# Kernel optimization log

Hardware: AMD Instinct MI355X
Metric: run time of the kernel (lower is better)

The kernel has to match this reference:

```python
import jax, jax.numpy as jnp
import numpy as np

WS = (4, 4, 4)  # window shape (wd, wh, ww)
EPS = 1e-5


def _layernorm(x, g, b):
    mu = jnp.mean(x, axis=-1, keepdims=True)
    var = jnp.mean(jnp.square(x - mu), axis=-1, keepdims=True)
    return (x - mu) * jax.lax.rsqrt(var + EPS) * g + b


def _partition(x, ws):
    # x: [B, D, H, W, C] -> [num_windows, wd*wh*ww, C]
    B, D, H, W, C = x.shape
    x = x.reshape(B, D // ws[0], ws[0], H // ws[1], ws[1], W // ws[2], ws[2], C)
    x = jnp.transpose(x, (0, 1, 3, 5, 2, 4, 6, 7))
    return x.reshape(-1, ws[0] * ws[1] * ws[2], C)


def _merge(win, shape, ws):
    B, D, H, W, C = shape
    x = win.reshape(B, D // ws[0], H // ws[1], W // ws[2], ws[0], ws[1], ws[2], C)
    x = jnp.transpose(x, (0, 1, 4, 2, 5, 3, 6, 7))
    return x.reshape(B, D, H, W, C)


def setup_inputs() -> dict:
    key = jax.random.key(0)
    ks = jax.random.split(key, 8)
    B, D, H, W, C = 2, 32, 64, 64, 96
    nh, kd = 4, 24
    s = 0.02
    return {
        "x": jax.random.normal(ks[0], (B, D, H, W, C), jnp.float32),
        "ln1_g": jnp.ones((C,), jnp.float32),
        "ln1_b": jnp.zeros((C,), jnp.float32),
        "wq": jax.random.normal(ks[1], (C, nh, kd), jnp.float32) * s,
        "bq": jnp.zeros((nh, kd), jnp.float32),
        "wk": jax.random.normal(ks[2], (C, nh, kd), jnp.float32) * s,
        "bk": jnp.zeros((nh, kd), jnp.float32),
        "wv": jax.random.normal(ks[3], (C, nh, kd), jnp.float32) * s,
        "bv": jnp.zeros((nh, kd), jnp.float32),
        "wo": jax.random.normal(ks[4], (nh, kd, C), jnp.float32) * s,
        "bo": jnp.zeros((C,), jnp.float32),
        "ln2_g": jnp.ones((C,), jnp.float32),
        "ln2_b": jnp.zeros((C,), jnp.float32),
        "w1": jax.random.normal(ks[5], (C, 4 * C), jnp.float32) * s,
        "b1": jnp.zeros((4 * C,), jnp.float32),
        "w2": jax.random.normal(ks[6], (4 * C, C), jnp.float32) * s,
        "b2": jnp.zeros((C,), jnp.float32),
    }


def reference(x, ln1_g, ln1_b, wq, bq, wk, bk, wv, bv, wo, bo,
              ln2_g, ln2_b, w1, b1, w2, b2):
    shape = x.shape  # [B, D, H, W, C]; dims chosen divisible by WS -> pad is a no-op
    kd = wq.shape[-1]
    shortcut = x
    h = _layernorm(x, ln1_g, ln1_b)
    win = _partition(h, WS)  # [n, L, C], L = 64
    # Keras MultiHeadAttention (inference, dropout off)
    q = jnp.einsum("nlc,chd->nlhd", win, wq) + bq
    k = jnp.einsum("nlc,chd->nlhd", win, wk) + bk
    v = jnp.einsum("nlc,chd->nlhd", win, wv) + bv
    scores = jnp.einsum("nlhd,nmhd->nhlm", q, k) / jnp.sqrt(jnp.float32(kd))
    attn = jax.nn.softmax(scores, axis=-1)
    o = jnp.einsum("nhlm,nmhd->nlhd", attn, v)
    out = jnp.einsum("nlhd,hdc->nlc", o, wo) + bo
    x = shortcut + _merge(out, shape, WS)
    shortcut = x
    h = _layernorm(x, ln2_g, ln2_b)
    h = jax.nn.gelu(h @ w1 + b1, approximate=False)  # TF keras 'gelu' is exact
    h = h @ w2 + b2
    return shortcut + h
```

## Files before the change

### kernel.cpp

```cpp
#include <hip/hip_runtime.h>
#include <hip/hip_bf16.h>

typedef __attribute__((ext_vector_type(8))) short short8;
typedef __attribute__((ext_vector_type(4))) short short4b;
typedef __attribute__((ext_vector_type(4))) float f32x4;
typedef unsigned short ushort_t;

#define NTOK 262144

__device__ __forceinline__ ushort_t f2bf(float f){
  __hip_bfloat16 h = __float2bfloat16(f);
  return *reinterpret_cast<ushort_t*>(&h);
}
__device__ __forceinline__ float bf2f(ushort_t u){
  union { unsigned int i; float f; } v; v.i = ((unsigned int)u) << 16; return v.f;
}
__device__ __forceinline__ float fast_rcp(float x){
  float r; asm("v_rcp_f32 %0, %1" : "=v"(r) : "v"(x)); return r;
}
__device__ __forceinline__ float gelu_f(float x){
  float e = __expf(-1.702f * x);
  return x * fast_rcp(1.0f + e);
}
__device__ __forceinline__ void bar_lds(){
  asm volatile("s_waitcnt lgkmcnt(0)" ::: "memory");
  __builtin_amdgcn_s_barrier();
  __builtin_amdgcn_sched_barrier(0);
}
__device__ __forceinline__ void bar_cnt5(){
  asm volatile("s_waitcnt vmcnt(5) lgkmcnt(0)" ::: "memory");
  __builtin_amdgcn_s_barrier();
  __builtin_amdgcn_sched_barrier(0);
}
__device__ __forceinline__ void bar_cnt0(){
  asm volatile("s_waitcnt vmcnt(0) lgkmcnt(0)" ::: "memory");
  __builtin_amdgcn_s_barrier();
  __builtin_amdgcn_sched_barrier(0);
}
__device__ __forceinline__ void gl_lds16(const ushort_t* g, ushort_t* l){
  __builtin_amdgcn_global_load_lds(
      (const __attribute__((address_space(1))) void*)g,
      (__attribute__((address_space(3))) void*)l, 16, 0, 0);
}

template<int NT>
__device__ __forceinline__ void stage_w(const ushort_t* __restrict__ src,
                                        int src_stride, ushort_t (*dst)[104], int tid)
{
  #pragma unroll
  for (int it = 0; it < (1248 + NT - 1) / NT; ++it) {
    int u = tid + it * NT;
    if (u < 1248) {
      int row = u / 13, c16 = u % 13;
      const ushort_t* sp = src + row * src_stride + ((c16 == 12) ? 0 : c16 * 8);
      gl_lds16(sp, &dst[0][0] + (size_t)(u & ~63) * 8);
    }
  }
}

__device__ __forceinline__ void stage_wp(const ushort_t* __restrict__ src,
                                         int src_stride, ushort_t* __restrict__ dst, int tid)
{
  #pragma unroll
  for (int it = 0; it < 5; ++it) {
    int u = tid + it * 256;
    int row = u / 13, c16 = u % 13;
    const ushort_t* sp = src + row * src_stride + ((c16 >= 12) ? 0 : c16 * 8);
    gl_lds16(sp, dst + (size_t)(u & ~63) * 8);
  }
}

__global__ __launch_bounds__(256) void prep_kernel(
    const float* __restrict__ wq, const float* __restrict__ wk, const float* __restrict__ wv,
    const float* __restrict__ wo, const float* __restrict__ w1, const float* __restrict__ w2,
    const float* __restrict__ bq, const float* __restrict__ bk, const float* __restrict__ bv,
    ushort_t* __restrict__ Wqkv, ushort_t* __restrict__ Wo,
    ushort_t* __restrict__ W1, ushort_t* __restrict__ W2, float* __restrict__ biasq)
{
  const float qs = 0.20412414523193150818f;
  int i = blockIdx.x * 256 + threadIdx.x;
  if (i < 27648) {
    int j = i / 96, c = i % 96;
    int s = j / 96, rem = j % 96;
    const float* src = (s == 0) ? wq : (s == 1) ? wk : wv;
    float val = src[c * 96 + rem];
    if (s == 0) val *= qs;
    Wqkv[j * 96 + c] = f2bf(val);
  } else if (i < 36864) {
    int ii = i - 27648;
    int c = ii / 96, hd = ii % 96;
    Wo[ii] = f2bf(wo[hd * 96 + c]);
  } else if (i < 73728) {
    int ii = i - 36864;
    int j = ii / 96, c = ii % 96;
    W1[ii] = f2bf(w1[c * 384 + j]);
  } else if (i < 110592) {
    int ii = i - 73728;
    int c = ii / 384, j = ii % 384;
    W2[ii] = f2bf(w2[j * 96 + c]);
  } else if (i < 110880) {
    int j = i - 110592;
    int s = j / 96, rem = j % 96;
    const float* src = (s == 0) ? bq : (s == 1) ? bk : bv;
    float val = src[rem];
    if (s == 0) val *= qs;
    biasq[j] = val;
  }
}

__global__ __launch_bounds__(256, 2) void fat_kernel(
    const float* __restrict__ x, const float* __restrict__ g, const float* __restrict__ b,
    const ushort_t* __restrict__ Wqkv, const float* __restrict__ biasq,
    const ushort_t* __restrict__ Wo, const float* __restrict__ bo,
    ushort_t* __restrict__ x2b)
{
  __shared__ ushort_t regionA[20480];
  __shared__ ushort_t Vt[4][32][72];
  __shared__ ushort_t Ws[96][104];
  ushort_t (*hbt)[104]   = reinterpret_cast<ushort_t(*)[104]>(regionA);
  ushort_t (*QK)[216]    = reinterpret_cast<ushort_t(*)[216]>(regionA + 64 * 104);
  ushort_t (*Pb)[64][72] = reinterpret_cast<ushort_t(*)[64][72]>(regionA);
  ushort_t (*O_lds)[104] = reinterpret_cast<ushort_t(*)[104]>(regionA);

  int tid = threadIdx.x;
  int n = blockIdx.x;
  int wq_ = n & 15, hq = (n >> 4) & 15, rest = n >> 8;
  int dq = rest & 7, bb_ = rest >> 3;
  int base = bb_ * 131072 + dq * 16384 + hq * 256 + wq_ * 4;
  #define TOK(s) (base + ((s) >> 4) * 4096 + (((s) >> 2) & 3) * 64 + ((s) & 3))

  stage_w<256>(Wqkv, 96, Ws, tid);

  {
    int s = tid >> 2, qr = tid & 3;
    const float* xp = x + (size_t)TOK(s) * 96 + qr * 24;
    f32x4 v[6];
    float sm = 0.f, sq = 0.f;
    #pragma unroll
    for (int i = 0; i < 6; i++) {
      v[i] = *reinterpret_cast<const f32x4*>(xp + i * 4);
      #pragma unroll
      for (int j = 0; j < 4; j++) { sm += v[i][j]; sq += v[i][j] * v[i][j]; }
    }
    sm += __shfl_xor(sm, 1); sq += __shfl_xor(sq, 1);
    sm += __shfl_xor(sm, 2); sq += __shfl_xor(sq, 2);
    float mean = sm * (1.0f / 96.0f);
    float var  = sq * (1.0f / 96.0f) - mean * mean;
    float rstd = rsqrtf(var + 1e-5f);
    #pragma unroll
    for (int i8 = 0; i8 < 3; i8++) {
      short8 pk;
      #pragma unroll
      for (int j = 0; j < 8; j++) {
        int c = qr * 24 + i8 * 8 + j;
        pk[j] = (short)f2bf((v[(i8 * 8 + j) >> 2][(i8 * 8 + j) & 3] - mean) * rstd * g[c] + b[c]);
      }
      *reinterpret_cast<short8*>(&hbt[s][qr * 24 + i8 * 8]) = pk;
    }
  }
  __syncthreads();

  int w = tid >> 6, lane = tid & 63, g16 = lane >> 4, l15 = lane & 15;
  short8 af[3];
  #pragma unroll
  for (int ks = 0; ks < 3; ks++)
    af[ks] = *reinterpret_cast<const short8*>(&hbt[w * 16 + l15][ks * 32 + g16 * 8]);

  for (int grp = 0; grp < 3; ++grp) {
    f32x4 acc[6];
    #pragma unroll
    for (int j = 0; j < 6; j++) acc[j] = (f32x4){0.f, 0.f, 0.f, 0.f};
    __builtin_amdgcn_s_setprio(1);
    #pragma unroll
    for (int j = 0; j < 6; j++)
      #pragma unroll
      for (int ks = 0; ks < 3; ks++) {
        short8 wfr = *reinterpret_cast<const short8*>(&Ws[j * 16 + l15][ks * 32 + g16 * 8]);
        acc[j] = __builtin_amdgcn_mfma_f32_16x16x32_bf16(wfr, af[ks], acc[j], 0, 0, 0);
      }
    __builtin_amdgcn_s_setprio(0);
    bar_lds();
    if (grp < 2) stage_w<256>(Wqkv + (grp + 1) * 9216, 96, Ws, tid);
    else         stage_w<256>(Wo, 96, Ws, tid);
    if (grp < 2) {
      #pragma unroll
      for (int j = 0; j < 6; j++) {
        int c0 = grp * 96 + j * 16 + g16 * 4;
        f32x4 bb4 = *reinterpret_cast<const f32x4*>(&biasq[c0]);
        unsigned lo = (unsigned)f2bf(acc[j][0] + bb4[0]) | ((unsigned)f2bf(acc[j][1] + bb4[1]) << 16);
        unsigned hi = (unsigned)f2bf(acc[j][2] + bb4[2]) | ((unsigned)f2bf(acc[j][3] + bb4[3]) << 16);
        uint2 pk; pk.x = lo; pk.y = hi;
        *reinterpret_cast<uint2*>(&QK[w * 16 + l15][c0]) = pk;
      }
    } else {
      #pragma unroll
      for (int j = 0; j < 6; j++) {
        int c0 = j * 16 + g16 * 4;
        f32x4 bb4 = *reinterpret_cast<const f32x4*>(&biasq[192 + c0]);
        #pragma unroll
        for (int r = 0; r < 4; r++) {
          int vcol = c0 + r;
          int h2 = vcol / 24, d2 = vcol - h2 * 24;
          Vt[h2][d2][w * 16 + l15] = f2bf(acc[j][r] + bb4[r]);
        }
      }
    }
    __syncthreads();
  }

  int h = w;
  short8 kf[4], qf[4];
  const short8 z8 = {0, 0, 0, 0, 0, 0, 0, 0};
  #pragma unroll
  for (int i = 0; i < 4; i++) {
    qf[i] = (g16 < 3) ? *(const short8*)&QK[i * 16 + l15][h * 24 + g16 * 8]      : z8;
    kf[i] = (g16 < 3) ? *(const short8*)&QK[i * 16 + l15][96 + h * 24 + g16 * 8] : z8;
  }
  f32x4 st[4][4];
  __builtin_amdgcn_s_setprio(1);
  #pragma unroll
  for (int tm = 0; tm < 4; tm++)
    #pragma unroll
    for (int tn = 0; tn < 4; tn++)
      st[tm][tn] = __builtin_amdgcn_mfma_f32_16x16x32_bf16(kf[tm], qf[tn],
                    (f32x4){0.f, 0.f, 0.f, 0.f}, 0, 0, 0);
  __builtin_amdgcn_s_setprio(0);
  bar_lds();

  #pragma unroll
  for (int tn = 0; tn < 4; tn++) {
    float m = st[0][tn][0];
    #pragma unroll
    for (int tm = 0; tm < 4; tm++)
      #pragma unroll
      for (int r = 0; r < 4; r++) m = fmaxf(m, st[tm][tn][r]);
    m = fmaxf(m, __shfl_xor(m, 16));
    m = fmaxf(m, __shfl_xor(m, 32));
    float sum = 0.f;
    #pragma unroll
    for (int tm = 0; tm < 4; tm++)
      #pragma unroll
      for (int r = 0; r < 4; r++) {
        float e = __expf(st[tm][tn][r] - m);
        st[tm][tn][r] = e;
        sum += e;
      }
    sum += __shfl_xor(sum, 16);
    sum += __shfl_xor(sum, 32);
    float inv = fast_rcp(sum);
    int q = tn * 16 + l15;
    #pragma unroll
    for (int tm = 0; tm < 4; tm++) {
      unsigned lo = (unsigned)f2bf(st[tm][tn][0] * inv) | ((unsigned)f2bf(st[tm][tn][1] * inv) << 16);
      unsigned hi = (unsigned)f2bf(st[tm][tn][2] * inv) | ((unsigned)f2bf(st[tm][tn][3] * inv) << 16);
      uint2 pk; pk.x = lo; pk.y = hi;
      *(uint2*)&Pb[h][q][tm * 16 + g16 * 4] = pk;
    }
  }

  f32x4 oacc[4][2];
  #pragma unroll
  for (int qt = 0; qt < 4; qt++)
    #pragma unroll
    for (int dt = 0; dt < 2; dt++) oacc[qt][dt] = (f32x4){0.f, 0.f, 0.f, 0.f};
  __builtin_amdgcn_s_setprio(1);
  #pragma unroll
  for (int ks = 0; ks < 2; ks++) {
    short8 vb[2];
    #pragma unroll
    for (int dt = 0; dt < 2; dt++)
      vb[dt] = *(const short8*)&Vt[h][dt * 16 + l15][ks * 32 + g16 * 8];
    #pragma unroll
    for (int qt = 0; qt < 4; qt++) {
      short8 pa = *(const short8*)&Pb[h][qt * 16 + l15][ks * 32 + g16 * 8];
      #pragma unroll
      for (int dt = 0; dt < 2; dt++)
        oacc[qt][dt] = __builtin_amdgcn_mfma_f32_16x16x32_bf16(pa, vb[dt], oacc[qt][dt], 0, 0, 0);
    }
  }
  __builtin_amdgcn_s_setprio(0);

  __syncthreads();
  #pragma unroll
  for (int qt = 0; qt < 4; qt++)
    #pragma unroll
    for (int dt = 0; dt < 2; dt++) {
      int d = dt * 16 + l15;
      if (d < 24) {
        #pragma unroll
        for (int r = 0; r < 4; r++)
          O_lds[qt * 16 + g16 * 4 + r][h * 24 + d] = f2bf(oacc[qt][dt][r]);
      }
    }
  __syncthreads();

  f32x4 pacc[6];
  #pragma unroll
  for (int nt = 0; nt < 6; nt++) pacc[nt] = (f32x4){0.f, 0.f, 0.f, 0.f};
  __builtin_amdgcn_s_setprio(1);
  #pragma unroll
  for (int ks = 0; ks < 3; ks++) {
    short8 pa = *(const short8*)&O_lds[w * 16 + l15][ks * 32 + g16 * 8];
    #pragma unroll
    for (int nt = 0; nt < 6; nt++) {
      short8 wb = *reinterpret_cast<const short8*>(&Ws[nt * 16 + l15][ks * 32 + g16 * 8]);
      pacc[nt] = __builtin_amdgcn_mfma_f32_16x16x32_bf16(wb, pa, pacc[nt], 0, 0, 0);
    }
  }
  __builtin_amdgcn_s_setprio(0);
  {
    size_t t = (size_t)TOK(w * 16 + l15);
    #pragma unroll
    for (int nt = 0; nt < 6; nt++) {
      int c0 = nt * 16 + g16 * 4;
      f32x4 bo4 = *reinterpret_cast<const f32x4*>(&bo[c0]);
      f32x4 xr  = *reinterpret_cast<const f32x4*>(&x[t * 96 + c0]);
      float v0 = pacc[nt][0] + bo4[0] + xr[0];
      float v1 = pacc[nt][1] + bo4[1] + xr[1];
      float v2 = pacc[nt][2] + bo4[2] + xr[2];
      float v3 = pacc[nt][3] + bo4[3] + xr[3];
      unsigned lo = (unsigned)f2bf(v0) | ((unsigned)f2bf(v1) << 16);
      unsigned hi = (unsigned)f2bf(v2) | ((unsigned)f2bf(v3) << 16);
      uint2 pk; pk.x = lo; pk.y = hi;
      *reinterpret_cast<uint2*>(&x2b[t * 96 + c0]) = pk;
    }
  }
  #undef TOK
}

__device__ __forceinline__ void ln_to_lds_b(const ushort_t* __restrict__ xrow_base,
    const float* __restrict__ gg, const float* __restrict__ bb,
    ushort_t (*hbt)[104], int tid)
{
  int row = tid >> 1, half = tid & 1;
  const ushort_t* xp = xrow_base + (size_t)row * 96 + half * 48;
  short8 vv[6];
  #pragma unroll
  for (int i = 0; i < 6; i++) vv[i] = *reinterpret_cast<const short8*>(xp + i * 8);
  float v[48];
  float s = 0.f, sq = 0.f;
  #pragma unroll
  for (int i = 0; i < 6; i++)
    #pragma unroll
    for (int j = 0; j < 8; j++) {
      float f = bf2f((ushort_t)vv[i][j]);
      v[i * 8 + j] = f; s += f; sq += f * f;
    }
  s  += __shfl_xor(s, 1);
  sq += __shfl_xor(sq, 1);
  float mean = s * (1.0f / 96.0f);
  float var  = sq * (1.0f / 96.0f) - mean * mean;
  float rstd = rsqrtf(var + 1e-5f);
  #pragma unroll
  for (int i8 = 0; i8 < 6; i8++) {
    short8 pk;
    #pragma unroll
    for (int j = 0; j < 8; j++) {
      int c = half * 48 + i8 * 8 + j;
      pk[j] = (short)f2bf((v[i8 * 8 + j] - mean) * rstd * gg[c] + bb[c]);
    }
    *reinterpret_cast<short8*>(&hbt[row][half * 48 + i8 * 8]) = pk;
  }
}

__global__ __launch_bounds__(256, 2) void mlp2_kernel(
    const ushort_t* __restrict__ x2b, const float* __restrict__ g, const float* __restrict__ b,
    const ushort_t* __restrict__ W1t, const float* __restrict__ b1,
    const ushort_t* __restrict__ W2t, const float* __restrict__ b2,
    float* __restrict__ out)
{
  __shared__ ushort_t smem[128][104];
  __shared__ ushort_t WsA[10240];
  __shared__ ushort_t WsB[10240];
  __shared__ float bias1[384];
  __shared__ float bias2[96];
  int tid = threadIdx.x;
  size_t r0 = (size_t)blockIdx.x * 128;

  stage_wp(W1t, 96, WsA, tid);
  stage_wp(W2t, 384, WsB, tid);
  bias1[tid] = b1[tid];
  if (tid < 128) bias1[256 + tid] = b1[256 + tid];
  if (tid < 96)  bias2[tid] = b2[tid];
  ln_to_lds_b(x2b + r0 * 96, g, b, smem, tid);

  int w = tid >> 6, lane = tid & 63, g16 = lane >> 4, l15 = lane & 15;
  short8 af[2][3];
  #pragma unroll
  for (int mi = 0; mi < 2; mi++)
    #pragma unroll
    for (int ks = 0; ks < 3; ks++)
      af[mi][ks] = *reinterpret_cast<const short8*>(&smem[w * 32 + mi * 16 + l15][ks * 32 + g16 * 8]);
  __builtin_amdgcn_sched_barrier(0);

  f32x4 oacc[6][2];
  #pragma unroll
  for (int nt = 0; nt < 6; nt++) { oacc[nt][0] = (f32x4){0.f,0.f,0.f,0.f}; oacc[nt][1] = (f32x4){0.f,0.f,0.f,0.f}; }

  for (int cc = 0; cc < 4; ++cc) {
    bar_cnt5();
    f32x4 acc[6][2];
    #pragma unroll
    for (int nt = 0; nt < 6; nt++) { acc[nt][0] = (f32x4){0.f,0.f,0.f,0.f}; acc[nt][1] = (f32x4){0.f,0.f,0.f,0.f}; }
    __builtin_amdgcn_s_setprio(1);
    #pragma unroll
    for (int nt = 0; nt < 6; nt++)
      #pragma unroll
      for (int ks = 0; ks < 3; ks++) {
        short8 wfr = *reinterpret_cast<const short8*>(&WsA[(nt * 16 + l15) * 104 + ks * 32 + g16 * 8]);
        acc[nt][0] = __builtin_amdgcn_mfma_f32_16x16x32_bf16(wfr, af[0][ks], acc[nt][0], 0, 0, 0);
        acc[nt][1] = __builtin_amdgcn_mfma_f32_16x16x32_bf16(wfr, af[1][ks], acc[nt][1], 0, 0, 0);
      }
    __builtin_amdgcn_s_setprio(0);
    #pragma unroll
    for (int nt = 0; nt < 6; nt++) {
      f32x4 bb4 = *reinterpret_cast<const f32x4*>(&bias1[cc * 96 + nt * 16 + g16 * 4]);
      #pragma unroll
      for (int mi = 0; mi < 2; mi++) {
        float g0 = gelu_f(acc[nt][mi][0] + bb4[0]);
        float g1 = gelu_f(acc[nt][mi][1] + bb4[1]);
        float g2 = gelu_f(acc[nt][mi][2] + bb4[2]);
        float g3 = gelu_f(acc[nt][mi][3] + bb4[3]);
        unsigned lo = (unsigned)f2bf(g0) | ((unsigned)f2bf(g1) << 16);
        unsigned hi = (unsigned)f2bf(g2) | ((unsigned)f2bf(g3) << 16);
        uint2 pk; pk.x = lo; pk.y = hi;
        *reinterpret_cast<uint2*>(&smem[w * 32 + mi * 16 + l15][nt * 16 + g16 * 4]) = pk;
      }
    }
    short8 a2[2][3];
    #pragma unroll
    for (int mi = 0; mi < 2; mi++)
      #pragma unroll
      for (int ks = 0; ks < 3; ks++)
        a2[mi][ks] = *reinterpret_cast<const short8*>(&smem[w * 32 + mi * 16 + l15][ks * 32 + g16 * 8]);
    bar_lds();
    if (cc < 3) stage_wp(W1t + (cc + 1) * 9216, 96, WsA, tid);
    if (cc < 3) bar_cnt5(); else bar_cnt0();
    __builtin_amdgcn_s_setprio(1);
    #pragma unroll
    for (int nt = 0; nt < 6; nt++)
      #pragma unroll
      for (int ks = 0; ks < 3; ks++) {
        short8 wfr = *reinterpret_cast<const short8*>(&WsB[(nt * 16 + l15) * 104 + ks * 32 + g16 * 8]);
        oacc[nt][0] = __builtin_amdgcn_mfma_f32_16x16x32_bf16(wfr, a2[0][ks], oacc[nt][0], 0, 0, 0);
        oacc[nt][1] = __builtin_amdgcn_mfma_f32_16x16x32_bf16(wfr, a2[1][ks], oacc[nt][1], 0, 0, 0);
      }
    __builtin_amdgcn_s_setprio(0);
    if (cc < 3) {
      bar_lds();
      stage_wp(W2t + (cc + 1) * 96, 384, WsB, tid);
    }
  }

  #pragma unroll
  for (int nt = 0; nt < 6; nt++) {
    int c0 = nt * 16 + g16 * 4;
    f32x4 bb4 = *reinterpret_cast<const f32x4*>(&bias2[c0]);
    #pragma unroll
    for (int mi = 0; mi < 2; mi++) {
      size_t row = r0 + w * 32 + mi * 16 + l15;
      short4b rr = *reinterpret_cast<const short4b*>(&x2b[row * 96 + c0]);
      f32x4 o;
      #pragma unroll
      for (int r = 0; r < 4; r++) o[r] = oacc[nt][mi][r] + bb4[r] + bf2f((ushort_t)rr[r]);
      *reinterpret_cast<f32x4*>(&out[row * 96 + c0]) = o;
    }
  }
}

extern "C" void kernel_launch(void* const* d_in, const int* in_sizes, int n_in,
                              void* d_out, int out_size, void* d_ws, size_t ws_size,
                              hipStream_t stream)
{
  (void)in_sizes; (void)n_in; (void)out_size; (void)ws_size;
  const float* x    = (const float*)d_in[0];
  const float* ln1g = (const float*)d_in[1];
  const float* ln1b = (const float*)d_in[2];
  const float* wq   = (const float*)d_in[3];
  const float* bq   = (const float*)d_in[4];
  const float* wk   = (const float*)d_in[5];
  const float* bk   = (const float*)d_in[6];
  const float* wv   = (const float*)d_in[7];
  const float* bv   = (const float*)d_in[8];
  const float* wo   = (const float*)d_in[9];
  const float* bo   = (const float*)d_in[10];
  const float* ln2g = (const float*)d_in[11];
  const float* ln2b = (const float*)d_in[12];
  const float* w1   = (const float*)d_in[13];
  const float* b1   = (const float*)d_in[14];
  const float* w2   = (const float*)d_in[15];
  const float* b2   = (const float*)d_in[16];

  char* ws = (char*)d_ws;
  ushort_t* x2b  = (ushort_t*)(ws);
  char* wsw      = ws + 50331648;
  ushort_t* Wqkv = (ushort_t*)(wsw);
  ushort_t* Wo   = (ushort_t*)(wsw + 55296);
  ushort_t* W1   = (ushort_t*)(wsw + 55296 + 18432);
  ushort_t* W2   = (ushort_t*)(wsw + 55296 + 18432 + 73728);
  float*    biasq= (float*)   (wsw + 55296 + 18432 + 73728 + 73728);

  prep_kernel<<<434, 256, 0, stream>>>(wq, wk, wv, wo, w1, w2, bq, bk, bv,
                                       Wqkv, Wo, W1, W2, biasq);
  fat_kernel<<<4096, 256, 0, stream>>>(x, ln1g, ln1b, Wqkv, biasq, Wo, bo, x2b);
  mlp2_kernel<<<NTOK / 128, 256, 0, stream>>>(x2b, ln2g, ln2b, W1, b1, W2, b2, (float*)d_out);
}
```

Measured before the change: 183.3 us.

## Double-buffer QKV/Wo weight halves in LDS with vmcnt-based pipelined staging

Replaces the single padded 96x104 weight tile with two unpadded 48x96 half-tile buffers. Each half is staged with global_load_lds two steps ahead and waited on with a partial vmcnt barrier, so weight loads overlap the QKV projection MFMAs. It also drops the initial __syncthreads after LayerNorm, makes QK alias hbt in a smaller region, and swaps some __syncthreads for lighter custom barriers. Removing the padding may bring LDS bank conflicts on fragment reads. The hbt/QK aliasing and the counter-based waits are fragile correctness points.

```diff
diff --git a/kernel.cpp b/kernel.cpp
--- a/kernel.cpp
+++ b/kernel.cpp
@@ -27,6 +27,11 @@
   __builtin_amdgcn_s_barrier();
   __builtin_amdgcn_sched_barrier(0);
 }
+__device__ __forceinline__ void bar_cnt2(){
+  asm volatile("s_waitcnt vmcnt(2) lgkmcnt(0)" ::: "memory");
+  __builtin_amdgcn_s_barrier();
+  __builtin_amdgcn_sched_barrier(0);
+}
 __device__ __forceinline__ void bar_cnt5(){
   asm volatile("s_waitcnt vmcnt(5) lgkmcnt(0)" ::: "memory");
   __builtin_amdgcn_s_barrier();
@@ -43,19 +48,13 @@
       (__attribute__((address_space(3))) void*)l, 16, 0, 0);
 }
 
-template<int NT>
-__device__ __forceinline__ void stage_w(const ushort_t* __restrict__ src,
-                                        int src_stride, ushort_t (*dst)[104], int tid)
-{
-  #pragma unroll
-  for (int it = 0; it < (1248 + NT - 1) / NT; ++it) {
-    int u = tid + it * NT;
-    if (u < 1248) {
-      int row = u / 13, c16 = u % 13;
-      const ushort_t* sp = src + row * src_stride + ((c16 == 12) ? 0 : c16 * 8);
-      gl_lds16(sp, &dst[0][0] + (size_t)(u & ~63) * 8);
-    }
-  }
+__device__ __forceinline__ void stage_half(const ushort_t* __restrict__ src,
+                                           ushort_t* __restrict__ dst, int tid)
+{
+  gl_lds16(src + (size_t)tid * 8, dst + (size_t)(tid & ~63) * 8);
+  gl_lds16(src + (size_t)(tid + 256) * 8, dst + (size_t)((tid + 256) & ~63) * 8);
+  if (tid < 64)
+    gl_lds16(src + (size_t)(tid + 512) * 8, dst + (size_t)512 * 8);
 }
 
 __device__ __forceinline__ void stage_wp(const ushort_t* __restrict__ src,
@@ -114,11 +113,11 @@
     const ushort_t* __restrict__ Wo, const float* __restrict__ bo,
     ushort_t* __restrict__ x2b)
 {
-  __shared__ ushort_t regionA[20480];
+  __shared__ ushort_t regionA[18432];
   __shared__ ushort_t Vt[4][32][72];
-  __shared__ ushort_t Ws[96][104];
+  __shared__ ushort_t WsH[2][4608];
   ushort_t (*hbt)[104]   = reinterpret_cast<ushort_t(*)[104]>(regionA);
-  ushort_t (*QK)[216]    = reinterpret_cast<ushort_t(*)[216]>(regionA + 64 * 104);
+  ushort_t (*QK)[200]    = reinterpret_cast<ushort_t(*)[200]>(regionA);
   ushort_t (*Pb)[64][72] = reinterpret_cast<ushort_t(*)[64][72]>(regionA);
   ushort_t (*O_lds)[104] = reinterpret_cast<ushort_t(*)[104]>(regionA);
 
@@ -129,7 +128,8 @@
   int base = bb_ * 131072 + dq * 16384 + hq * 256 + wq_ * 4;
   #define TOK(s) (base + ((s) >> 4) * 4096 + (((s) >> 2) & 3) * 64 + ((s) & 3))
 
-  stage_w<256>(Wqkv, 96, Ws, tid);
+  stage_half(Wqkv, WsH[0], tid);
+  stage_half(Wqkv + 4608, WsH[1], tid);
 
   {
     int s = tid >> 2, qr = tid & 3;
@@ -158,55 +158,64 @@
       *reinterpret_cast<short8*>(&hbt[s][qr * 24 + i8 * 8]) = pk;
     }
   }
-  __syncthreads();
 
   int w = tid >> 6, lane = tid & 63, g16 = lane >> 4, l15 = lane & 15;
   short8 af[3];
   #pragma unroll
   for (int ks = 0; ks < 3; ks++)
     af[ks] = *reinterpret_cast<const short8*>(&hbt[w * 16 + l15][ks * 32 + g16 * 8]);
-
+  __builtin_amdgcn_sched_barrier(0);
+
+  int hidx = 0;
   for (int grp = 0; grp < 3; ++grp) {
-    f32x4 acc[6];
-    #pragma unroll
-    for (int j = 0; j < 6; j++) acc[j] = (f32x4){0.f, 0.f, 0.f, 0.f};
-    __builtin_amdgcn_s_setprio(1);
-    #pragma unroll
-    for (int j = 0; j < 6; j++)
-      #pragma unroll
-      for (int ks = 0; ks < 3; ks++) {
-        short8 wfr = *reinterpret_cast<const short8*>(&Ws[j * 16 + l15][ks * 32 + g16 * 8]);
-        acc[j] = __builtin_amdgcn_mfma_f32_16x16x32_bf16(wfr, af[ks], acc[j], 0, 0, 0);
-      }
-    __builtin_amdgcn_s_setprio(0);
-    bar_lds();
-    if (grp < 2) stage_w<256>(Wqkv + (grp + 1) * 9216, 96, Ws, tid);
-    else         stage_w<256>(Wo, 96, Ws, tid);
-    if (grp < 2) {
-      #pragma unroll
-      for (int j = 0; j < 6; j++) {
-        int c0 = grp * 96 + j * 16 + g16 * 4;
-        f32x4 bb4 = *reinterpret_cast<const f32x4*>(&biasq[c0]);
-        unsigned lo = (unsigned)f2bf(acc[j][0] + bb4[0]) | ((unsigned)f2bf(acc[j][1] + bb4[1]) << 16);
-        unsigned hi = (unsigned)f2bf(acc[j][2] + bb4[2]) | ((unsigned)f2bf(acc[j][3] + bb4[3]) << 16);
-        uint2 pk; pk.x = lo; pk.y = hi;
-        *reinterpret_cast<uint2*>(&QK[w * 16 + l15][c0]) = pk;
-      }
-    } else {
-      #pragma unroll
-      for (int j = 0; j < 6; j++) {
-        int c0 = j * 16 + g16 * 4;
-        f32x4 bb4 = *reinterpret_cast<const f32x4*>(&biasq[192 + c0]);
+    for (int half = 0; half < 2; ++half) {
+      const ushort_t* buf = WsH[hidx & 1];
+      bar_cnt2();
+      f32x4 acc[3];
+      #pragma unroll
+      for (int jj = 0; jj < 3; jj++) acc[jj] = (f32x4){0.f, 0.f, 0.f, 0.f};
+      __builtin_amdgcn_s_setprio(1);
+      #pragma unroll
+      for (int jj = 0; jj < 3; jj++)
         #pragma unroll
-        for (int r = 0; r < 4; r++) {
-          int vcol = c0 + r;
-          int h2 = vcol / 24, d2 = vcol - h2 * 24;
-          Vt[h2][d2][w * 16 + l15] = f2bf(acc[j][r] + bb4[r]);
+        for (int ks = 0; ks < 3; ks++) {
+          short8 wfr = *reinterpret_cast<const short8*>(&buf[(jj * 16 + l15) * 96 + ks * 32 + g16 * 8]);
+          acc[jj] = __builtin_amdgcn_mfma_f32_16x16x32_bf16(wfr, af[ks], acc[jj], 0, 0, 0);
         }
-      }
-    }
-    __syncthreads();
-  }
+      __builtin_amdgcn_s_setprio(0);
+      bar_lds();
+      if (hidx < 6) {
+        const ushort_t* s2 = (hidx + 2 < 6) ? Wqkv + (size_t)(hidx + 2) * 4608
+                                            : Wo + (size_t)(hidx - 4) * 4608;
+        stage_half(s2, WsH[hidx & 1], tid);
+      }
+      if (grp < 2) {
+        #pragma unroll
+        for (int jj = 0; jj < 3; jj++) {
+          int c0 = grp * 96 + (half * 3 + jj) * 16 + g16 * 4;
+          f32x4 bb4 = *reinterpret_cast<const f32x4*>(&biasq[c0]);
+          unsigned lo = (unsigned)f2bf(acc[jj][0] + bb4[0]) | ((unsigned)f2bf(acc[jj][1] + bb4[1]) << 16);
+          unsigned hi = (unsigned)f2bf(acc[jj][2] + bb4[2]) | ((unsigned)f2bf(acc[jj][3] + bb4[3]) << 16);
+          uint2 pk; pk.x = lo; pk.y = hi;
+          *reinterpret_cast<uint2*>(&QK[w * 16 + l15][c0]) = pk;
+        }
+      } else {
+        #pragma unroll
+        for (int jj = 0; jj < 3; jj++) {
+          int c0 = (half * 3 + jj) * 16 + g16 * 4;
+          f32x4 bb4 = *reinterpret_cast<const f32x4*>(&biasq[192 + c0]);
+          #pragma unroll
+          for (int r = 0; r < 4; r++) {
+            int vcol = c0 + r;
+            int h2 = vcol / 24, d2 = vcol - h2 * 24;
+            Vt[h2][d2][w * 16 + l15] = f2bf(acc[jj][r] + bb4[r]);
+          }
+        }
+      }
+      hidx++;
+    }
+  }
+  bar_lds();
 
   int h = w;
   short8 kf[4], qf[4];
@@ -280,7 +289,7 @@
   }
   __builtin_amdgcn_s_setprio(0);
 
-  __syncthreads();
+  bar_lds();
   #pragma unroll
   for (int qt = 0; qt < 4; qt++)
     #pragma unroll
@@ -292,7 +301,7 @@
           O_lds[qt * 16 + g16 * 4 + r][h * 24 + d] = f2bf(oacc[qt][dt][r]);
       }
     }
-  __syncthreads();
+  bar_cnt0();
 
   f32x4 pacc[6];
   #pragma unroll
@@ -303,7 +312,8 @@
     short8 pa = *(const short8*)&O_lds[w * 16 + l15][ks * 32 + g16 * 8];
     #pragma unroll
     for (int nt = 0; nt < 6; nt++) {
-      short8 wb = *reinterpret_cast<const short8*>(&Ws[nt * 16 + l15][ks * 32 + g16 * 8]);
+      const ushort_t* buf = WsH[(nt < 3) ? 0 : 1];
+      short8 wb = *reinterpret_cast<const short8*>(&buf[((nt % 3) * 16 + l15) * 96 + ks * 32 + g16 * 8]);
       pacc[nt] = __builtin_amdgcn_mfma_f32_16x16x32_bf16(wb, pa, pacc[nt], 0, 0, 0);
     }
   }
```

New measurement: 187.5 us. 2.3% more time.
